# Kernel optimization log

Hardware: AMD Instinct MI355X
Metric: run time of the kernel (lower is better)

The kernel has to match this reference:

```python
import jax, jax.numpy as jnp
import numpy as np

B, L, H, P = 4, 8192, 256, 256


def discretize(log_real, imag, log_Delta, B_real, B_imag):
    # Lambda = -exp(log_real) + i*imag ; ZOH discretization
    Lr = -jnp.exp(log_real)
    Li = imag
    Delta = jnp.exp(log_Delta)
    ad = Lr * Delta
    bd = Li * Delta
    exp_ad = jnp.exp(ad)
    Lbar_r = exp_ad * jnp.cos(bd)
    Lbar_i = exp_ad * jnp.sin(bd)
    denom = jnp.maximum(Lr * Lr + Li * Li, 1e-12)
    inv_Lr = Lr / denom
    inv_Li = -Li / denom
    diff_r = Lbar_r - 1.0
    diff_i = Lbar_i
    coeff_r = inv_Lr * diff_r - inv_Li * diff_i
    coeff_i = inv_Lr * diff_i + inv_Li * diff_r
    B_bar_r = coeff_r[:, None] * B_real - coeff_i[:, None] * B_imag
    B_bar_i = coeff_r[:, None] * B_imag + coeff_i[:, None] * B_real
    return Lbar_r, Lbar_i, B_bar_r, B_bar_i


def binop(ei, ej):
    Ar_i, Ai_i, xr_i, xi_i = ei
    Ar_j, Ai_j, xr_j, xi_j = ej
    return (Ar_j * Ar_i - Ai_j * Ai_i,
            Ar_j * Ai_i + Ai_j * Ar_i,
            Ar_j * xr_i - Ai_j * xi_i + xr_j,
            Ar_j * xi_i + Ai_j * xr_i + xi_j)


def apply_ssm(Lbar_r, Lbar_i, B_bar_r, B_bar_i, C_real, C_imag, D, x):
    # x: (B,L,H), B_bar: (P,H), C: (H,P)
    Bu_r = jnp.einsum('blh,ph->blp', x, B_bar_r)
    Bu_i = jnp.einsum('blh,ph->blp', x, B_bar_i)
    A_r = jnp.broadcast_to(Lbar_r, Bu_r.shape)
    A_i = jnp.broadcast_to(Lbar_i, Bu_i.shape)
    _, _, xs_r, xs_i = jax.lax.associative_scan(binop, (A_r, A_i, Bu_r, Bu_i), axis=1)
    ys = jnp.einsum('blp,hp->blh', xs_r, C_real) - jnp.einsum('blp,hp->blh', xs_i, C_imag)
    return ys + D * x


def s5(log_real, imag, log_Delta, B_real, B_imag, C_real, C_imag, D, x):
    Lbar_r, Lbar_i, B_bar_r, B_bar_i = discretize(log_real, imag, log_Delta, B_real, B_imag)
    y = apply_ssm(Lbar_r, Lbar_i, B_bar_r, B_bar_i, C_real, C_imag, D, x)
    return jax.nn.gelu(y, approximate=False)


def setup_inputs() -> dict:
    key = jax.random.key(0)
    ks = jax.random.split(key, 17)
    std_b = 1.0 / H ** 0.5
    std_c = 1.0 / P ** 0.5
    def params(ki):
        k = jax.random.split(ks[ki], 8)
        return dict(
            log_real=jax.random.normal(k[0], (P,), jnp.float32) * 0.5,
            imag=jax.random.normal(k[1], (P,), jnp.float32),
            log_Delta=jnp.zeros((P,), jnp.float32),
            B_real=jax.random.normal(k[2], (P, H), jnp.float32) * std_b,
            B_imag=jax.random.normal(k[3], (P, H), jnp.float32) * std_b,
            C_real=jax.random.normal(k[4], (H, P), jnp.float32) * std_c,
            C_imag=jax.random.normal(k[5], (H, P), jnp.float32) * std_c,
            D=jnp.ones((H,), jnp.float32),
        )
    f = params(1)
    b = params(2)
    inp = {'x': jax.random.normal(ks[0], (B, L, H), jnp.float32)}
    for name, v in f.items():
        inp['fwd_' + name] = v
    for name, v in b.items():
        inp['bwd_' + name] = v
    return inp


def reference(x,
              fwd_log_real, fwd_imag, fwd_log_Delta, fwd_B_real, fwd_B_imag,
              fwd_C_real, fwd_C_imag, fwd_D,
              bwd_log_real, bwd_imag, bwd_log_Delta, bwd_B_real, bwd_B_imag,
              bwd_C_real, bwd_C_imag, bwd_D):
    x_flip = jnp.flip(x, axis=1)
    y_f = s5(fwd_log_real, fwd_imag, fwd_log_Delta, fwd_B_real, fwd_B_imag,
             fwd_C_real, fwd_C_imag, fwd_D, x)
    y_b = s5(bwd_log_real, bwd_imag, bwd_log_Delta, bwd_B_real, bwd_B_imag,
             bwd_C_real, bwd_C_imag, bwd_D, x_flip)
    return y_f + jnp.flip(y_b, axis=1)
```

## Files before the change

kernel.cpp:

```cpp
#include <hip/hip_runtime.h>
#include <math.h>

#define B_DIM 4
#define L_DIM 8192
#define H_DIM 256
#define P_DIM 256
#define M_DIM (B_DIM * L_DIM)
#define NC 64
#define LC 128

typedef __attribute__((ext_vector_type(8))) short bf16x8;
typedef __attribute__((ext_vector_type(4))) float f32x4;

static __device__ __forceinline__ float bf2f(unsigned int u) {
    union { unsigned int i; float f; } v; v.i = u << 16; return v.f;
}
static __device__ __forceinline__ unsigned short f2bf(float f) {
    union { float f; unsigned int i; } v; v.f = f;
    unsigned int r = v.i + 0x7FFFu + ((v.i >> 16) & 1u);
    return (unsigned short)(r >> 16);
}
static __device__ __forceinline__ float gelu_f(float x) {
    float z = 0.7978845608028654f * (x + 0.044715f * x * x * x);
    float e = __expf(2.0f * z);
    float t = 1.0f - 2.0f / (e + 1.0f);
    return 0.5f * x * (1.0f + t);
}
static __device__ __forceinline__ void async_load16(const void* g, void* l) {
    __builtin_amdgcn_global_load_lds(
        (const __attribute__((address_space(1))) unsigned int*)g,
        (__attribute__((address_space(3))) unsigned int*)l, 16, 0, 0);
}

__global__ void prep_kernel(const float* fLr, const float* fIm, const float* fLd,
                            const float* fBr, const float* fBi,
                            const float* fCr, const float* fCi,
                            const float* bLr, const float* bIm, const float* bLd,
                            const float* bBr, const float* bBi,
                            const float* bCr, const float* bCi,
                            unsigned short* Bmat, unsigned short* B3, float2* LbarWS) {
    int gid = blockIdx.x * 256 + threadIdx.x;
    if (gid < 262144) {
        int k = gid >> 8, h = gid & 255;
        int d = k >> 9, pc = k & 511, p = pc >> 1, comp = pc & 1;
        const float* LR = d ? bLr : fLr;
        const float* IM = d ? bIm : fIm;
        const float* LD = d ? bLd : fLd;
        const float* BR = d ? bBr : fBr;
        const float* BI = d ? bBi : fBi;
        float Lr = -expf(LR[p]);
        float Li = IM[p];
        float Delta = expf(LD[p]);
        float ea = expf(Lr * Delta);
        float bd = Li * Delta;
        float Lbr = ea * cosf(bd);
        float Lbi = ea * sinf(bd);
        float denom = fmaxf(Lr * Lr + Li * Li, 1e-12f);
        float ivr = Lr / denom, ivi = -Li / denom;
        float dr = Lbr - 1.0f, di = Lbi;
        float cr = ivr * dr - ivi * di;
        float ci = ivr * di + ivi * dr;
        float br = BR[p * 256 + h], bi = BI[p * 256 + h];
        float val = comp ? (cr * bi + ci * br) : (cr * br - ci * bi);
        Bmat[gid] = f2bf(val);
    } else if (gid < 524288) {
        int g2 = gid - 262144;
        int d = g2 >> 17;
        int rem = g2 & 131071;
        int h = rem >> 9;
        int kk = rem & 511;
        int p = kk >> 1, comp = kk & 1;
        const float* CR = d ? bCr : fCr;
        const float* CI = d ? bCi : fCi;
        float val = comp ? -CI[h * 256 + p] : CR[h * 256 + p];
        B3[g2] = f2bf(val);
    } else if (gid < 524800) {
        int g2 = gid - 524288;
        int d = g2 >> 8, p = g2 & 255;
        const float* LR = d ? bLr : fLr;
        const float* IM = d ? bIm : fIm;
        const float* LD = d ? bLd : fLd;
        float Lr = -expf(LR[p]); float Li = IM[p]; float Delta = expf(LD[p]);
        float ea = expf(Lr * Delta); float bd = Li * Delta;
        LbarWS[g2] = make_float2(ea * cosf(bd), ea * sinf(bd));
    }
}

__global__ void xcast_kernel(const float4* __restrict__ x4, ushort4* __restrict__ xb) {
    int gid = blockIdx.x * 256 + threadIdx.x;
    float4 v = x4[gid];
    ushort4 o;
    o.x = f2bf(v.x); o.y = f2bf(v.y); o.z = f2bf(v.z); o.w = f2bf(v.w);
    xb[gid] = o;
}

__global__ __launch_bounds__(256, 2) void k1_gemm(const unsigned short* __restrict__ A,
                                                  const unsigned short* __restrict__ Bm,
                                                  unsigned short* __restrict__ Bu,
                                                  const float2* __restrict__ Lbar,
                                                  float2* __restrict__ carry) {
    __shared__ unsigned short SH[16384];
    __shared__ float2 Sbuf[64];
    int tid = threadIdx.x;
    int lane = tid & 63, wv = tid >> 6;
    int wm = (wv >> 1) * 64, wn = (wv & 1) * 64;
    int Mb = blockIdx.x * 128, Nb = blockIdx.y * 128;
    int lr = lane >> 3;
    int swz = ((lane & 7) ^ lr) * 8;
    f32x4 acc[4][4];
#pragma unroll
    for (int i = 0; i < 4; i++)
#pragma unroll
        for (int j = 0; j < 4; j++) acc[i][j] = (f32x4){0.f, 0.f, 0.f, 0.f};
    int mrow = lane & 15, quad = lane >> 4;
    for (int kb = 0; kb < 256; kb += 64) {
#pragma unroll
        for (int ch = wv; ch < 16; ch += 4) {
            int r = ch * 8 + lr;
            async_load16(A  + (size_t)(Mb + r) * 256 + kb + swz, (char*)SH + ch * 1024);
            async_load16(Bm + (size_t)(Nb + r) * 256 + kb + swz, (char*)SH + 16384 + ch * 1024);
        }
        __syncthreads();
#pragma unroll
        for (int kk = 0; kk < 64; kk += 32) {
            bf16x8 af[4], bfr[4];
#pragma unroll
            for (int i = 0; i < 4; i++) {
                int rr = wm + 16 * i + mrow;
                af[i] = *(const bf16x8*)&SH[rr * 64 + ((((kk >> 3) + quad) ^ (rr & 7)) << 3)];
            }
#pragma unroll
            for (int j = 0; j < 4; j++) {
                int rr = wn + 16 * j + mrow;
                bfr[j] = *(const bf16x8*)&SH[8192 + rr * 64 + ((((kk >> 3) + quad) ^ (rr & 7)) << 3)];
            }
#pragma unroll
            for (int i = 0; i < 4; i++)
#pragma unroll
                for (int j = 0; j < 4; j++)
                    acc[i][j] = __builtin_amdgcn_mfma_f32_16x16x32_bf16(af[i], bfr[j], acc[i][j], 0, 0, 0);
        }
        __syncthreads();
    }
    unsigned short* Cs = SH;
#pragma unroll
    for (int i = 0; i < 4; i++)
#pragma unroll
        for (int j = 0; j < 4; j++)
#pragma unroll
            for (int r = 0; r < 4; r++) {
                int row = wm + 16 * i + quad * 4 + r;
                int col = wn + 16 * j + mrow;
                Cs[row * 128 + col] = f2bf(acc[i][j][r]);
            }
    __syncthreads();
#pragma unroll
    for (int it = 0; it < 8; it++) {
        int o = tid * 16 + it * 4096;
        int row = o >> 8, colb = o & 255;
        uint4 v = *(const uint4*)((const char*)Cs + o);
        *(uint4*)((char*)Bu + (size_t)(Mb + row) * 2048 + (size_t)Nb * 2 + colb) = v;
    }
    int d = Nb >> 9;
    int b = Mb >> 13;
    int c = (Mb >> 7) & 63;
    float sr = 0.f, si = 0.f;
    float2 A2 = make_float2(0.f, 0.f);
    int p = 0;
    if (tid < 128) {
        int j = tid & 63, half = tid >> 6;
        p = ((Nb & 511) >> 1) + j;
        A2 = Lbar[d * 256 + p];
        const unsigned int* C32 = (const unsigned int*)Cs;
        int r0 = half * 64;
        if (d == 0) {
            for (int t = 0; t < 64; t++) {
                unsigned int v = C32[(r0 + t) * 64 + j];
                float zr = bf2f(v & 0xffffu), zi = bf2f(v >> 16);
                float nr = A2.x * sr - A2.y * si + zr;
                float ni = A2.x * si + A2.y * sr + zi;
                sr = nr; si = ni;
            }
        } else {
            for (int t = 63; t >= 0; t--) {
                unsigned int v = C32[(r0 + t) * 64 + j];
                float zr = bf2f(v & 0xffffu), zi = bf2f(v >> 16);
                float nr = A2.x * sr - A2.y * si + zr;
                float ni = A2.x * si + A2.y * sr + zi;
                sr = nr; si = ni;
            }
        }
        if (half == 1) Sbuf[j] = make_float2(sr, si);
    }
    __syncthreads();
    if (tid < 64) {
        float2 S1 = Sbuf[tid];
        float a64r = A2.x, a64i = A2.y;
#pragma unroll
        for (int k = 0; k < 6; k++) {
            float nr = a64r * a64r - a64i * a64i;
            float ni = 2.f * a64r * a64i;
            a64r = nr; a64i = ni;
        }
        float cr, ci;
        if (d == 0) {
            cr = a64r * sr - a64i * si + S1.x;
            ci = a64r * si + a64i * sr + S1.y;
        } else {
            cr = sr + a64r * S1.x - a64i * S1.y;
            ci = si + a64r * S1.y + a64i * S1.x;
        }
        carry[((size_t)(d * 4 + b) * NC + c) * 256 + p] = make_float2(cr, ci);
    }
}

__global__ __launch_bounds__(512) void scan_fix_kernel(unsigned int* __restrict__ XSu,
                                                       const float2* __restrict__ Lbar,
                                                       const float2* __restrict__ carry) {
    int c = blockIdx.x, b = blockIdx.y;
    int d = threadIdx.x >> 8;
    int p = threadIdx.x & 255;
    float2 A = Lbar[d * 256 + p];
    float ar = A.x, ai = A.y;
    float a128r = ar, a128i = ai;
#pragma unroll
    for (int k = 0; k < 7; k++) {
        float nr = a128r * a128r - a128i * a128i;
        float ni = 2.f * a128r * a128i;
        a128r = nr; a128i = ni;
    }
    float sr = 0.f, si = 0.f;
    const float2* cb = carry + ((size_t)(d * 4 + b) * NC) * 256 + p;
    size_t base = (size_t)b * L_DIM * 512 + d * 256 + p;
    if (d == 0) {
        for (int j = 0; j < c; j++) {
            float2 cj = cb[(size_t)j * 256];
            float nr = a128r * sr - a128i * si + cj.x;
            float ni = a128r * si + a128i * sr + cj.y;
            sr = nr; si = ni;
        }
#pragma unroll 16
        for (int t = 0; t < LC; t++) {
            size_t idx = base + (size_t)(c * LC + t) * 512;
            unsigned int v = XSu[idx];
            float zr = bf2f(v & 0xffffu), zi = bf2f(v >> 16);
            float nr = ar * sr - ai * si + zr;
            float ni = ar * si + ai * sr + zi;
            sr = nr; si = ni;
            XSu[idx] = (unsigned int)f2bf(sr) | ((unsigned int)f2bf(si) << 16);
        }
    } else {
        for (int j = NC - 1; j > c; j--) {
            float2 cj = cb[(size_t)j * 256];
            float nr = a128r * sr - a128i * si + cj.x;
            float ni = a128r * si + a128i * sr + cj.y;
            sr = nr; si = ni;
        }
#pragma unroll 16
        for (int t = LC - 1; t >= 0; t--) {
            size_t idx = base + (size_t)(c * LC + t) * 512;
            unsigned int v = XSu[idx];
            float zr = bf2f(v & 0xffffu), zi = bf2f(v >> 16);
            float nr = ar * sr - ai * si + zr;
            float ni = ar * si + ai * sr + zi;
            sr = nr; si = ni;
            XSu[idx] = (unsigned int)f2bf(sr) | ((unsigned int)f2bf(si) << 16);
        }
    }
}

static __device__ __forceinline__ void k3_half(const unsigned short* __restrict__ XS,
                                               const unsigned short* __restrict__ B3h,
                                               unsigned short* As, unsigned short* Bs,
                                               int Mb, int Hb, int coff,
                                               int wm, int wn, int mrow, int quad,
                                               int lr, int swz, int wv,
                                               f32x4 (&acc)[4][4]) {
    for (int kb = 0; kb < 512; kb += 64) {
#pragma unroll
        for (int ch = wv; ch < 16; ch += 4) {
            int r = ch * 8 + lr;
            async_load16(XS + (size_t)(Mb + r) * 1024 + coff + kb + swz, (char*)As + ch * 1024);
            async_load16(B3h + (size_t)(Hb + r) * 512 + kb + swz, (char*)Bs + ch * 1024);
        }
        __syncthreads();
#pragma unroll
        for (int kk = 0; kk < 64; kk += 32) {
            bf16x8 af[4], bfr[4];
#pragma unroll
            for (int i = 0; i < 4; i++) {
                int rr = wm + 16 * i + mrow;
                af[i] = *(const bf16x8*)&As[rr * 64 + ((((kk >> 3) + quad) ^ (rr & 7)) << 3)];
            }
#pragma unroll
            for (int j = 0; j < 4; j++) {
                int rr = wn + 16 * j + mrow;
                bfr[j] = *(const bf16x8*)&Bs[rr * 64 + ((((kk >> 3) + quad) ^ (rr & 7)) << 3)];
            }
#pragma unroll
            for (int i = 0; i < 4; i++)
#pragma unroll
                for (int j = 0; j < 4; j++)
                    acc[i][j] = __builtin_amdgcn_mfma_f32_16x16x32_bf16(af[i], bfr[j], acc[i][j], 0, 0, 0);
        }
        __syncthreads();
    }
}

__global__ __launch_bounds__(256, 2) void k3_gemm(const unsigned short* __restrict__ XS,
                                                  const unsigned short* __restrict__ B3,
                                                  const unsigned short* __restrict__ xbf,
                                                  const float* __restrict__ Df,
                                                  const float* __restrict__ Db,
                                                  float* __restrict__ out) {
    __shared__ unsigned short As[128 * 64];
    __shared__ unsigned short Bs[128 * 64];
    int tid = threadIdx.x;
    int lane = tid & 63, wv = tid >> 6;
    int wm = (wv >> 1) * 64, wn = (wv & 1) * 64;
    int Mb = blockIdx.x * 128, Hb = blockIdx.y * 128;
    int lr = lane >> 3;
    int swz = ((lane & 7) ^ lr) * 8;
    int mrow = lane & 15, quad = lane >> 4;
    f32x4 accf[4][4], accb[4][4];
#pragma unroll
    for (int i = 0; i < 4; i++)
#pragma unroll
        for (int j = 0; j < 4; j++) {
            accf[i][j] = (f32x4){0.f, 0.f, 0.f, 0.f};
            accb[i][j] = (f32x4){0.f, 0.f, 0.f, 0.f};
        }
    k3_half(XS, B3,          As, Bs, Mb, Hb, 0,   wm, wn, mrow, quad, lr, swz, wv, accf);
    k3_half(XS, B3 + 131072, As, Bs, Mb, Hb, 512, wm, wn, mrow, quad, lr, swz, wv, accb);
#pragma unroll
    for (int i = 0; i < 4; i++)
#pragma unroll
        for (int j = 0; j < 4; j++) {
            int h = Hb + wn + 16 * j + mrow;
            float df = Df[h], db = Db[h];
#pragma unroll
            for (int r = 0; r < 4; r++) {
                int row = Mb + wm + 16 * i + quad * 4 + r;
                float xv = bf2f((unsigned int)xbf[(size_t)row * 256 + h]);
                float yf = accf[i][j][r] + df * xv;
                float yb = accb[i][j][r] + db * xv;
                out[(size_t)row * 256 + h] = gelu_f(yf) + gelu_f(yb);
            }
        }
}

extern "C" void kernel_launch(void* const* d_in, const int* in_sizes, int n_in,
                              void* d_out, int out_size, void* d_ws, size_t ws_size,
                              hipStream_t stream) {
    const float* x   = (const float*)d_in[0];
    const float* fLr = (const float*)d_in[1];
    const float* fIm = (const float*)d_in[2];
    const float* fLd = (const float*)d_in[3];
    const float* fBr = (const float*)d_in[4];
    const float* fBi = (const float*)d_in[5];
    const float* fCr = (const float*)d_in[6];
    const float* fCi = (const float*)d_in[7];
    const float* fD  = (const float*)d_in[8];
    const float* bLr = (const float*)d_in[9];
    const float* bIm = (const float*)d_in[10];
    const float* bLd = (const float*)d_in[11];
    const float* bBr = (const float*)d_in[12];
    const float* bBi = (const float*)d_in[13];
    const float* bCr = (const float*)d_in[14];
    const float* bCi = (const float*)d_in[15];
    const float* bD  = (const float*)d_in[16];
    float* out = (float*)d_out;

    char* ws = (char*)d_ws;
    unsigned short* xbf  = (unsigned short*)(ws);
    unsigned short* Bu   = (unsigned short*)(ws + 16777216);
    unsigned short* Bmat = (unsigned short*)(ws + 16777216 + 67108864);
    unsigned short* B3   = (unsigned short*)(ws + 16777216 + 67108864 + 524288);
    float2* LbarWS = (float2*)(ws + 16777216 + 67108864 + 1048576);
    float2* carry  = (float2*)(ws + 16777216 + 67108864 + 1048576 + 4096);

    prep_kernel<<<2050, 256, 0, stream>>>(fLr, fIm, fLd, fBr, fBi, fCr, fCi,
                                          bLr, bIm, bLd, bBr, bBi, bCr, bCi,
                                          Bmat, B3, LbarWS);
    xcast_kernel<<<8192, 256, 0, stream>>>((const float4*)x, (ushort4*)xbf);
    k1_gemm<<<dim3(256, 8), 256, 0, stream>>>(xbf, Bmat, Bu, LbarWS, carry);
    scan_fix_kernel<<<dim3(NC, 4), 512, 0, stream>>>((unsigned int*)Bu, LbarWS, carry);
    k3_gemm<<<dim3(256, 2), 256, 0, stream>>>(Bu, B3, xbf, fD, bD, out);
}
```

Baseline: 203.5 us.

## Split scan fixup into half-chunks using stored half carries; fuse x cast into prep

k1_gemm now also stores the 64-step half-chunk partial state, so scan_fix can launch twice as many blocks, each rescanning only 64 timesteps after applying the chunk and half-chunk carries. The aim is more parallelism in the latency-bound sequential fixup, which previously ran only 256 blocks. Separately, the x-to-bf16 cast is folded into prep_kernel to remove one kernel launch. The cost is an extra carry buffer write and read, plus one larger, more divergent prep grid.

```diff
diff --git a/kernel.cpp b/kernel.cpp
--- a/kernel.cpp
+++ b/kernel.cpp
@@ -38,10 +38,19 @@
                             const float* bLr, const float* bIm, const float* bLd,
                             const float* bBr, const float* bBi,
                             const float* bCr, const float* bCi,
+                            const float4* __restrict__ x4, ushort4* __restrict__ xb,
                             unsigned short* Bmat, unsigned short* B3, float2* LbarWS) {
     int gid = blockIdx.x * 256 + threadIdx.x;
-    if (gid < 262144) {
-        int k = gid >> 8, h = gid & 255;
+    if (gid < 2097152) {
+        float4 v = x4[gid];
+        ushort4 o;
+        o.x = f2bf(v.x); o.y = f2bf(v.y); o.z = f2bf(v.z); o.w = f2bf(v.w);
+        xb[gid] = o;
+        return;
+    }
+    int g1 = gid - 2097152;
+    if (g1 < 262144) {
+        int k = g1 >> 8, h = g1 & 255;
         int d = k >> 9, pc = k & 511, p = pc >> 1, comp = pc & 1;
         const float* LR = d ? bLr : fLr;
         const float* IM = d ? bIm : fIm;
@@ -62,9 +71,9 @@
         float ci = ivr * di + ivi * dr;
         float br = BR[p * 256 + h], bi = BI[p * 256 + h];
         float val = comp ? (cr * bi + ci * br) : (cr * br - ci * bi);
-        Bmat[gid] = f2bf(val);
-    } else if (gid < 524288) {
-        int g2 = gid - 262144;
+        Bmat[g1] = f2bf(val);
+    } else if (g1 < 524288) {
+        int g2 = g1 - 262144;
         int d = g2 >> 17;
         int rem = g2 & 131071;
         int h = rem >> 9;
@@ -74,8 +83,8 @@
         const float* CI = d ? bCi : fCi;
         float val = comp ? -CI[h * 256 + p] : CR[h * 256 + p];
         B3[g2] = f2bf(val);
-    } else if (gid < 524800) {
-        int g2 = gid - 524288;
+    } else if (g1 < 524800) {
+        int g2 = g1 - 524288;
         int d = g2 >> 8, p = g2 & 255;
         const float* LR = d ? bLr : fLr;
         const float* IM = d ? bIm : fIm;
@@ -86,19 +95,12 @@
     }
 }
 
-__global__ void xcast_kernel(const float4* __restrict__ x4, ushort4* __restrict__ xb) {
-    int gid = blockIdx.x * 256 + threadIdx.x;
-    float4 v = x4[gid];
-    ushort4 o;
-    o.x = f2bf(v.x); o.y = f2bf(v.y); o.z = f2bf(v.z); o.w = f2bf(v.w);
-    xb[gid] = o;
-}
-
 __global__ __launch_bounds__(256, 2) void k1_gemm(const unsigned short* __restrict__ A,
                                                   const unsigned short* __restrict__ Bm,
                                                   unsigned short* __restrict__ Bu,
                                                   const float2* __restrict__ Lbar,
-                                                  float2* __restrict__ carry) {
+                                                  float2* __restrict__ carry,
+                                                  float2* __restrict__ halfc) {
     __shared__ unsigned short SH[16384];
     __shared__ float2 Sbuf[64];
     int tid = threadIdx.x;
@@ -203,45 +205,79 @@
             a64r = nr; a64i = ni;
         }
         float cr, ci;
+        float2 hv;
         if (d == 0) {
             cr = a64r * sr - a64i * si + S1.x;
             ci = a64r * si + a64i * sr + S1.y;
+            hv = make_float2(sr, si);
         } else {
             cr = sr + a64r * S1.x - a64i * S1.y;
             ci = si + a64r * S1.y + a64i * S1.x;
-        }
-        carry[((size_t)(d * 4 + b) * NC + c) * 256 + p] = make_float2(cr, ci);
+            hv = S1;
+        }
+        size_t cidx = ((size_t)(d * 4 + b) * NC + c) * 256 + p;
+        carry[cidx] = make_float2(cr, ci);
+        halfc[cidx] = hv;
     }
 }
 
 __global__ __launch_bounds__(512) void scan_fix_kernel(unsigned int* __restrict__ XSu,
                                                        const float2* __restrict__ Lbar,
-                                                       const float2* __restrict__ carry) {
-    int c = blockIdx.x, b = blockIdx.y;
+                                                       const float2* __restrict__ carry,
+                                                       const float2* __restrict__ halfc) {
+    int m = blockIdx.x, b = blockIdx.y;
+    int c = m >> 1, h = m & 1;
     int d = threadIdx.x >> 8;
     int p = threadIdx.x & 255;
     float2 A = Lbar[d * 256 + p];
     float ar = A.x, ai = A.y;
-    float a128r = ar, a128i = ai;
-#pragma unroll
-    for (int k = 0; k < 7; k++) {
-        float nr = a128r * a128r - a128i * a128i;
-        float ni = 2.f * a128r * a128i;
-        a128r = nr; a128i = ni;
-    }
+    float a64r = ar, a64i = ai;
+#pragma unroll
+    for (int k = 0; k < 6; k++) {
+        float nr = a64r * a64r - a64i * a64i;
+        float ni = 2.f * a64r * a64i;
+        a64r = nr; a64i = ni;
+    }
+    float a128r = a64r * a64r - a64i * a64i;
+    float a128i = 2.f * a64r * a64i;
     float sr = 0.f, si = 0.f;
     const float2* cb = carry + ((size_t)(d * 4 + b) * NC) * 256 + p;
-    size_t base = (size_t)b * L_DIM * 512 + d * 256 + p;
+    size_t hidx = ((size_t)(d * 4 + b) * NC + c) * 256 + p;
     if (d == 0) {
+#pragma unroll 4
         for (int j = 0; j < c; j++) {
             float2 cj = cb[(size_t)j * 256];
             float nr = a128r * sr - a128i * si + cj.x;
             float ni = a128r * si + a128i * sr + cj.y;
             sr = nr; si = ni;
         }
+        if (h) {
+            float2 hc = halfc[hidx];
+            float nr = a64r * sr - a64i * si + hc.x;
+            float ni = a64r * si + a64i * sr + hc.y;
+            sr = nr; si = ni;
+        }
+    } else {
+#pragma unroll 4
+        for (int j = NC - 1; j > c; j--) {
+            float2 cj = cb[(size_t)j * 256];
+            float nr = a128r * sr - a128i * si + cj.x;
+            float ni = a128r * si + a128i * sr + cj.y;
+            sr = nr; si = ni;
+        }
+        if (!h) {
+            float2 hc = halfc[hidx];
+            float nr = a64r * sr - a64i * si + hc.x;
+            float ni = a64r * si + a64i * sr + hc.y;
+            sr = nr; si = ni;
+        }
+    }
+    size_t base = (size_t)b * L_DIM * 512 + d * 256 + p;
+    int l0 = c * 128 + h * 64;
+    if (d == 0) {
 #pragma unroll 16
-        for (int t = 0; t < LC; t++) {
-            size_t idx = base + (size_t)(c * LC + t) * 512;
+        for (int t = 0; t < 64; t++) {
+            size_t idx = base + (size_t)(l0 + t) * 512;
             unsigned int v = XSu[idx];
             float zr = bf2f(v & 0xffffu), zi = bf2f(v >> 16);
             float nr = ar * sr - ai * si + zr;
@@ -250,15 +286,9 @@
             XSu[idx] = (unsigned int)f2bf(sr) | ((unsigned int)f2bf(si) << 16);
         }
     } else {
-        for (int j = NC - 1; j > c; j--) {
-            float2 cj = cb[(size_t)j * 256];
-            float nr = a128r * sr - a128i * si + cj.x;
-            float ni = a128r * si + a128i * sr + cj.y;
-            sr = nr; si = ni;
-        }
 #pragma unroll 16
-        for (int t = LC - 1; t >= 0; t--) {
-            size_t idx = base + (size_t)(c * LC + t) * 512;
+        for (int t = 63; t >= 0; t--) {
+            size_t idx = base + (size_t)(l0 + t) * 512;
             unsigned int v = XSu[idx];
             float zr = bf2f(v & 0xffffu), zi = bf2f(v >> 16);
             float nr = ar * sr - ai * si + zr;
@@ -378,12 +408,13 @@
     unsigned short* B3   = (unsigned short*)(ws + 16777216 + 67108864 + 524288);
     float2* LbarWS = (float2*)(ws + 16777216 + 67108864 + 1048576);
     float2* carry  = (float2*)(ws + 16777216 + 67108864 + 1048576 + 4096);
-
-    prep_kernel<<<2050, 256, 0, stream>>>(fLr, fIm, fLd, fBr, fBi, fCr, fCi,
-                                          bLr, bIm, bLd, bBr, bBi, bCr, bCi,
-                                          Bmat, B3, LbarWS);
-    xcast_kernel<<<8192, 256, 0, stream>>>((const float4*)x, (ushort4*)xbf);
-    k1_gemm<<<dim3(256, 8), 256, 0, stream>>>(xbf, Bmat, Bu, LbarWS, carry);
-    scan_fix_kernel<<<dim3(NC, 4), 512, 0, stream>>>((unsigned int*)Bu, LbarWS, carry);
+    float2* halfc  = (float2*)(ws + 16777216 + 67108864 + 1048576 + 4096 + 1048576);
+
+    prep_kernel<<<10242, 256, 0, stream>>>(fLr, fIm, fLd, fBr, fBi, fCr, fCi,
+                                           bLr, bIm, bLd, bBr, bBi, bCr, bCi,
+                                           (const float4*)x, (ushort4*)xbf,
+                                           Bmat, B3, LbarWS);
+    k1_gemm<<<dim3(256, 8), 256, 0, stream>>>(xbf, Bmat, Bu, LbarWS, carry, halfc);
+    scan_fix_kernel<<<dim3(128, 4), 512, 0, stream>>>((unsigned int*)Bu, LbarWS, carry, halfc);
     k3_gemm<<<dim3(256, 2), 256, 0, stream>>>(Bu, B3, xbf, fD, bD, out);
 }
```

New measurement: 198.1 us. 1.03x faster.
